# Optimization experiments

Hardware: AMD Instinct MI355X
Metric: run time of the kernel (lower is better)

The kernel has to match this reference:

```python
import jax, jax.numpy as jnp
import numpy as np

VOCAB = 50000
E = 128      # embedding_dim (== hidden so layer weights stack)
H = 128      # hidden_features
L = 2        # n_layers
B = 256      # batch
T = 2048     # seq_len


def setup_inputs() -> dict:
    key = jax.random.key(0)
    ks = jax.random.split(key, 8)
    s = 1.0 / np.sqrt(H)
    x = jax.random.randint(ks[0], (B, T), 0, VOCAB)
    lengths = jax.random.randint(ks[1], (B,), 1, T + 1)
    emb = jax.random.normal(ks[2], (VOCAB, E), jnp.float32) * 0.1
    W_ih = jax.random.uniform(ks[3], (L, H, H), jnp.float32, -s, s)
    W_hh = jax.random.uniform(ks[4], (L, H, H), jnp.float32, -s, s)
    b = jax.random.uniform(ks[5], (L, H), jnp.float32, -s, s)
    cls_w = jax.random.uniform(ks[6], (H, 1), jnp.float32, -s, s)
    cls_b = jnp.zeros((1,), jnp.float32)
    return {"x": x, "lengths": lengths, "emb": emb, "W_ih": W_ih,
            "W_hh": W_hh, "b": b, "cls_w": cls_w, "cls_b": cls_b}


def reference(x, lengths, emb, W_ih, W_hh, b, cls_w, cls_b):
    # x: [B, T] right-padded token ids; lengths: [B] valid lengths.
    ex = emb[x]                       # [B, T, E]
    xs = jnp.moveaxis(ex, 1, 0)       # [T, B, E]
    seq = x.shape[1]
    mask = jnp.arange(seq)[:, None] < lengths[None, :]  # [T, B] alive at step t

    n_layers = W_ih.shape[0]

    def step(hid, inp):
        # hid: [L, B, H]; packed-RNN semantics: only alive rows update.
        tok, m = inp                  # [B, E], [B]
        h_in = tok
        new = []
        for l in range(n_layers):
            h = jnp.tanh(h_in @ W_ih[l] + hid[l] @ W_hh[l] + b[l])
            h = jnp.where(m[:, None], h, hid[l])
            new.append(h)
            h_in = h
        return jnp.stack(new), None

    hid0 = jnp.zeros((n_layers, x.shape[0], W_hh.shape[-1]), emb.dtype)
    hid, _ = jax.lax.scan(step, hid0, (xs, mask))
    # final hidden of last layer -> single-logit sigmoid classifier
    out = jax.nn.sigmoid(hid[-1] @ cls_w + cls_b)  # [B, 1]
    return out
```

## Files before the change

kernel.cpp:

```cpp
#include <hip/hip_runtime.h>
#include <math.h>

#define BATCH 256
#define SEQ   2048
#define HID   128
#define NTHR  256
#define VOCAB 50000

typedef _Float16 v2h __attribute__((ext_vector_type(2)));

template<int CTRL>
__device__ __forceinline__ float dpp_movf(float x) {
    return __builtin_bit_cast(float,
        __builtin_amdgcn_update_dpp(0, __builtin_bit_cast(int, x),
                                    CTRL, 0xF, 0xF, false));
}
__device__ __forceinline__ float quad_reduce(float x) {
    x += dpp_movf<0xB1>(x);
    x += dpp_movf<0x4E>(x);
    return x;
}
__device__ __forceinline__ float fast_rcp(float x) { return __builtin_amdgcn_rcpf(x); }
__device__ __forceinline__ float dot2(v2h a, v2h b, float c) {
    return __builtin_amdgcn_fdot2(a, b, c, false);
}
#define BCH(u) __builtin_bit_cast(v2h, (u))

__device__ __forceinline__ void barrier_lds() {
    asm volatile("s_waitcnt lgkmcnt(0)\n\ts_barrier" ::: "memory");
}

__global__ __launch_bounds__(512, 2) void emb_proj_kernel(
    const float* __restrict__ emb,
    const float* __restrict__ W_ih,
    const float* __restrict__ bias,
    _Float16*    __restrict__ Y)
{
    const int tid  = threadIdx.x;
    const int wave = tid >> 6;
    const int lane = tid & 63;
    const int j    = wave * 16 + (lane >> 2);
    const int q    = lane & 3;

    __shared__ __align__(16) _Float16 xr[HID];

    v2h w[16];
#pragma unroll
    for (int i = 0; i < 16; ++i) {
        const int k = q * 32 + 2 * i;
        w[i] = v2h{(_Float16)W_ih[k * HID + j], (_Float16)W_ih[(k + 1) * HID + j]};
    }
    const float bj = bias[j];
    const float4* embf4 = (const float4*)emb;

    for (int r = blockIdx.x; r < VOCAB; r += gridDim.x) {
        if (tid < 32) {
            float4 v = embf4[(size_t)r * 32 + tid];
            uint a01 = __builtin_bit_cast(uint, __builtin_amdgcn_cvt_pkrtz(v.x, v.y));
            uint a23 = __builtin_bit_cast(uint, __builtin_amdgcn_cvt_pkrtz(v.z, v.w));
            ((uint2*)&xr[0])[tid] = uint2{a01, a23};
        }
        __syncthreads();
        const uint4* xp = (const uint4*)&xr[0] + q * 4;
        float acc = 0.f;
#pragma unroll
        for (int i = 0; i < 4; ++i) {
            const uint4 xu = xp[i];
            acc = dot2(BCH(xu.x), w[4*i+0], acc);
            acc = dot2(BCH(xu.y), w[4*i+1], acc);
            acc = dot2(BCH(xu.z), w[4*i+2], acc);
            acc = dot2(BCH(xu.w), w[4*i+3], acc);
        }
        acc = quad_reduce(acc) + bj;
        if (q == 0) Y[(size_t)r * HID + j] = (_Float16)acc;
        __syncthreads();
    }
}

__global__ __launch_bounds__(NTHR, 1) void rnn_dot2_kernel(
    const int*      __restrict__ x,
    const int*      __restrict__ lengths,
    const _Float16* __restrict__ Y,
    const float*    __restrict__ W_ih,
    const float*    __restrict__ W_hh,
    const float*    __restrict__ bias,
    const float*    __restrict__ cls_w,
    const float*    __restrict__ cls_b,
    float*          __restrict__ out)
{
    const int b    = blockIdx.x;
    const int tid  = threadIdx.x;
    const int wave = tid >> 6;
    const int lane = tid & 63;
    const int jg   = wave * 16 + (lane >> 2);
    const int q    = lane & 3;
    const int jm   = lane & 1;
    const int isl1 = (lane >> 1) & 1;
    const int jt   = 2 * jg + jm;

    __shared__ int xids[SEQ];
    __shared__ __align__(16) _Float16 h0h[2][HID];
    __shared__ __align__(16) _Float16 h1h[2][HID];
    __shared__ __align__(16) float    red[HID];

    const int len   = lengths[b];
    const int lenm1 = len - 1;
    const float LOG2E2 = 2.88539008177793f;

    for (int i = tid; i < SEQ; i += NTHR) xids[i] = x[b * SEQ + i];
    if (tid < HID) {
        h0h[0][tid] = (_Float16)0.f; h0h[1][tid] = (_Float16)0.f;
        h1h[0][tid] = (_Float16)0.f; h1h[1][tid] = (_Float16)0.f;
    }

    v2h whh0[2][16], wih1[2][16], whh1[2][16];
#pragma unroll
    for (int i = 0; i < 16; ++i) {
        const int k = 32 * q + 2 * i;
#pragma unroll
        for (int m = 0; m < 2; ++m) {
            const int j = 2 * jg + m;
            whh0[m][i] = v2h{(_Float16)W_hh[k * HID + j],
                             (_Float16)W_hh[(k + 1) * HID + j]};
            wih1[m][i] = v2h{(_Float16)W_ih[HID * HID + k * HID + j],
                             (_Float16)W_ih[HID * HID + (k + 1) * HID + j]};
            whh1[m][i] = v2h{(_Float16)W_hh[HID * HID + k * HID + j],
                             (_Float16)W_hh[HID * HID + (k + 1) * HID + j]};
        }
    }
    const float b1K = bias[HID + jt] * LOG2E2;

    __syncthreads();

    _Float16 zA = Y[(size_t)xids[0] * HID + jt];
    _Float16 zB = Y[(size_t)xids[min(1, lenm1)] * HID + jt];

    int ph = 0, pf = 0;

#define TANH_PRE(ZK) (1.0f - 2.0f * fast_rcp(__builtin_amdgcn_exp2f(ZK) + 1.0f))

#define DO_PHASE(RD, WR, ZREG)                                              \
    {                                                                       \
        const uint4* h0p = (const uint4*)&h0h[RD][0] + q * 4;               \
        const uint4* h1p = (const uint4*)&h1h[RD][0] + q * 4;               \
        const float zcK = (float)ZREG * LOG2E2;                             \
        {                                                                   \
            const int tn = xids[min(ph + 2, lenm1)];                        \
            ZREG = Y[(size_t)tn * HID + jt];                                \
        }                                                                   \
        float a0_0 = 0.f, a0_1 = 0.f;             \
        float aA_0 = 0.f, aA_1 = 0.f;                        \
        float aB_0 = 0.f, aB_1 = 0.f;                        \
        _Pragma("unroll")                                                   \
        for (int c = 0; c < 4; ++c) {                                       \
            const uint4 hu = h0p[c];                                        \
            const uint4 gu = h1p[c];                                        \
            a0_0 = dot2(BCH(hu.x), whh0[0][4*c+0], a0_0);                   \
            a0_0 = dot2(BCH(hu.y), whh0[0][4*c+1], a0_0);                   \
            a0_0 = dot2(BCH(hu.z), whh0[0][4*c+2], a0_0);                   \
            a0_0 = dot2(BCH(hu.w), whh0[0][4*c+3], a0_0);                   \
            a0_1 = dot2(BCH(hu.x), whh0[1][4*c+0], a0_1);                   \
            a0_1 = dot2(BCH(hu.y), whh0[1][4*c+1], a0_1);                   \
            a0_1 = dot2(BCH(hu.z), whh0[1][4*c+2], a0_1);                   \
            a0_1 = dot2(BCH(hu.w), whh0[1][4*c+3], a0_1);                   \
            aA_0 = dot2(BCH(hu.x), wih1[0][4*c+0], aA_0);                   \
            aA_0 = dot2(BCH(hu.y), wih1[0][4*c+1], aA_0);                   \
            aA_0 = dot2(BCH(hu.z), wih1[0][4*c+2], aA_0);                   \
            aA_0 = dot2(BCH(hu.w), wih1[0][4*c+3], aA_0);                   \
            aA_1 = dot2(BCH(hu.x), wih1[1][4*c+0], aA_1);                   \
            aA_1 = dot2(BCH(hu.y), wih1[1][4*c+1], aA_1);                   \
            aA_1 = dot2(BCH(hu.z), wih1[1][4*c+2], aA_1);                   \
            aA_1 = dot2(BCH(hu.w), wih1[1][4*c+3], aA_1);                   \
            aB_0 = dot2(BCH(gu.x), whh1[0][4*c+0], aB_0);                   \
            aB_0 = dot2(BCH(gu.y), whh1[0][4*c+1], aB_0);                   \
            aB_0 = dot2(BCH(gu.z), whh1[0][4*c+2], aB_0);                   \
            aB_0 = dot2(BCH(gu.w), whh1[0][4*c+3], aB_0);                   \
            aB_1 = dot2(BCH(gu.x), whh1[1][4*c+0], aB_1);                   \
            aB_1 = dot2(BCH(gu.y), whh1[1][4*c+1], aB_1);                   \
            aB_1 = dot2(BCH(gu.z), whh1[1][4*c+2], aB_1);                   \
            aB_1 = dot2(BCH(gu.w), whh1[1][4*c+3], aB_1);                   \
        }                                                                   \
        float s0_0 = quad_reduce(a0_0);                                     \
        float s0_1 = quad_reduce(a0_1);                                     \
        float s1_0 = quad_reduce(aA_0 + aB_0);                              \
        float s1_1 = quad_reduce(aA_1 + aB_1);                              \
        const float sj  = jm  ? (isl1 ? s1_1 : s0_1) : (isl1 ? s1_0 : s0_0);\
        const float cj  = isl1 ? b1K : zcK;                                 \
        const float t   = TANH_PRE(__builtin_fmaf(sj, LOG2E2, cj));         \
        if (!isl1) { if (ph < len) h0h[WR][jt] = (_Float16)t; }             \
        else       { if (ph >= 1)  h1h[WR][jt] = (_Float16)t; }             \
        barrier_lds();                                                      \
    }

    for (;;) {
        DO_PHASE(0, 1, zA)
        ++ph;
        if (ph > len) { pf = 1; break; }
        DO_PHASE(1, 0, zB)
        ++ph;
        if (ph > len) { pf = 0; break; }
    }
#undef DO_PHASE
#undef TANH_PRE

    if (tid < HID) red[tid] = (float)h1h[pf][tid] * cls_w[tid];
    __syncthreads();
    if (tid == 0) {
        float s = 0.f;
        for (int i = 0; i < HID; ++i) s += red[i];
        s += cls_b[0];
        out[b] = fast_rcp(1.0f + __expf(-s));
    }
}

extern "C" void kernel_launch(void* const* d_in, const int* in_sizes, int n_in,
                              void* d_out, int out_size, void* d_ws, size_t ws_size,
                              hipStream_t stream) {
    const int*   x       = (const int*)  d_in[0];
    const int*   lengths = (const int*)  d_in[1];
    const float* emb     = (const float*)d_in[2];
    const float* W_ih    = (const float*)d_in[3];
    const float* W_hh    = (const float*)d_in[4];
    const float* bias    = (const float*)d_in[5];
    const float* cls_w   = (const float*)d_in[6];
    const float* cls_b   = (const float*)d_in[7];
    float*       out     = (float*)      d_out;

    _Float16* Yws = (_Float16*)d_ws;

    emb_proj_kernel<<<2048, 512, 0, stream>>>(emb, W_ih, bias, Yws);
    rnn_dot2_kernel<<<BATCH, NTHR, 0, stream>>>(
        x, lengths, Yws, W_ih, W_hh, bias, cls_w, cls_b, out);
}
```

Before: 834.7 us.

## Split RNN block into layer-0 and layer-1 wave groups with extra pipeline stage

```diff
diff --git a/kernel.cpp b/kernel.cpp
--- a/kernel.cpp
+++ b/kernel.cpp
@@ -4,7 +4,7 @@
 #define BATCH 256
 #define SEQ   2048
 #define HID   128
-#define NTHR  256
+#define NTHR  512
 #define VOCAB 50000
 
 typedef _Float16 v2h __attribute__((ext_vector_type(2)));
@@ -31,10 +31,8 @@
 }
 
 __global__ __launch_bounds__(512, 2) void emb_proj_kernel(
-    const float* __restrict__ emb,
-    const float* __restrict__ W_ih,
-    const float* __restrict__ bias,
-    _Float16*    __restrict__ Y)
+    const float* __restrict__ emb, const float* __restrict__ W_ih,
+    const float* __restrict__ bias, _Float16* __restrict__ Y)
 {
     const int tid  = threadIdx.x;
     const int wave = tid >> 6;
@@ -77,7 +75,7 @@
     }
 }
 
-__global__ __launch_bounds__(NTHR, 1) void rnn_dot2_kernel(
+__global__ __launch_bounds__(NTHR, 1) void rnn_split_kernel(
     const int*      __restrict__ x,
     const int*      __restrict__ lengths,
     const _Float16* __restrict__ Y,
@@ -92,117 +90,160 @@
     const int tid  = threadIdx.x;
     const int wave = tid >> 6;
     const int lane = tid & 63;
-    const int jg   = wave * 16 + (lane >> 2);
+    const bool isA = wave < 4;
+    const int wl   = isA ? wave : (wave - 4);
+    const int jg   = wl * 16 + (lane >> 2);
     const int q    = lane & 3;
     const int jm   = lane & 1;
-    const int isl1 = (lane >> 1) & 1;
+    const int sel  = (lane >> 1) & 1;
     const int jt   = 2 * jg + jm;
 
     __shared__ int xids[SEQ];
     __shared__ __align__(16) _Float16 h0h[2][HID];
     __shared__ __align__(16) _Float16 h1h[2][HID];
+    __shared__ __align__(16) float    gh[2][HID];
     __shared__ __align__(16) float    red[HID];
 
     const int len   = lengths[b];
     const int lenm1 = len - 1;
+    const int LIM   = len + 1;
     const float LOG2E2 = 2.88539008177793f;
 
     for (int i = tid; i < SEQ; i += NTHR) xids[i] = x[b * SEQ + i];
     if (tid < HID) {
         h0h[0][tid] = (_Float16)0.f; h0h[1][tid] = (_Float16)0.f;
         h1h[0][tid] = (_Float16)0.f; h1h[1][tid] = (_Float16)0.f;
-    }
-
-    v2h whh0[2][16], wih1[2][16], whh1[2][16];
-#pragma unroll
-    for (int i = 0; i < 16; ++i) {
-        const int k = 32 * q + 2 * i;
-#pragma unroll
-        for (int m = 0; m < 2; ++m) {
-            const int j = 2 * jg + m;
-            whh0[m][i] = v2h{(_Float16)W_hh[k * HID + j],
-                             (_Float16)W_hh[(k + 1) * HID + j]};
-            wih1[m][i] = v2h{(_Float16)W_ih[HID * HID + k * HID + j],
-                             (_Float16)W_ih[HID * HID + (k + 1) * HID + j]};
-            whh1[m][i] = v2h{(_Float16)W_hh[HID * HID + k * HID + j],
-                             (_Float16)W_hh[HID * HID + (k + 1) * HID + j]};
-        }
-    }
-    const float b1K = bias[HID + jt] * LOG2E2;
-
+        gh[0][tid]  = 0.f;           gh[1][tid]  = 0.f;
+    }
     __syncthreads();
 
-    _Float16 zA = Y[(size_t)xids[0] * HID + jt];
-    _Float16 zB = Y[(size_t)xids[min(1, lenm1)] * HID + jt];
-
     int ph = 0, pf = 0;
 
 #define TANH_PRE(ZK) (1.0f - 2.0f * fast_rcp(__builtin_amdgcn_exp2f(ZK) + 1.0f))
 
-#define DO_PHASE(RD, WR, ZREG)                                              \
+    if (isA) {
+        v2h whh0[2][16], wg[2][16];
+#pragma unroll
+        for (int i = 0; i < 16; ++i) {
+            const int k = 32 * q + 2 * i;
+#pragma unroll
+            for (int m = 0; m < 2; ++m) {
+                const int j = 2 * jg + m;
+                whh0[m][i] = v2h{(_Float16)W_hh[k * HID + j],
+                                 (_Float16)W_hh[(k + 1) * HID + j]};
+                wg[m][i]   = v2h{(_Float16)W_ih[HID * HID + k * HID + j],
+                                 (_Float16)W_ih[HID * HID + (k + 1) * HID + j]};
+            }
+        }
+        _Float16 zA = Y[(size_t)xids[0] * HID + jt];
+        _Float16 zB = Y[(size_t)xids[min(1, lenm1)] * HID + jt];
+
+#define A_PHASE(RD, WR, ZREG)                                               \
     {                                                                       \
         const uint4* h0p = (const uint4*)&h0h[RD][0] + q * 4;               \
-        const uint4* h1p = (const uint4*)&h1h[RD][0] + q * 4;               \
         const float zcK = (float)ZREG * LOG2E2;                             \
         {                                                                   \
             const int tn = xids[min(ph + 2, lenm1)];                        \
             ZREG = Y[(size_t)tn * HID + jt];                                \
         }                                                                   \
-        float a0_0 = 0.f, a0_1 = 0.f;             \
-        float aA_0 = 0.f, aA_1 = 0.f;                        \
-        float aB_0 = 0.f, aB_1 = 0.f;                        \
+        float a0 = 0.f, a1 = 0.f, g0 = 0.f, g1 = 0.f;                       \
         _Pragma("unroll")                                                   \
         for (int c = 0; c < 4; ++c) {                                       \
             const uint4 hu = h0p[c];                                        \
+            a0 = dot2(BCH(hu.x), whh0[0][4*c+0], a0);                       \
+            a0 = dot2(BCH(hu.y), whh0[0][4*c+1], a0);                       \
+            a0 = dot2(BCH(hu.z), whh0[0][4*c+2], a0);                       \
+            a0 = dot2(BCH(hu.w), whh0[0][4*c+3], a0);                       \
+            a1 = dot2(BCH(hu.x), whh0[1][4*c+0], a1);                       \
+            a1 = dot2(BCH(hu.y), whh0[1][4*c+1], a1);                       \
+            a1 = dot2(BCH(hu.z), whh0[1][4*c+2], a1);                       \
+            a1 = dot2(BCH(hu.w), whh0[1][4*c+3], a1);                       \
+            g0 = dot2(BCH(hu.x), wg[0][4*c+0], g0);                         \
+            g0 = dot2(BCH(hu.y), wg[0][4*c+1], g0);                         \
+            g0 = dot2(BCH(hu.z), wg[0][4*c+2], g0);                         \
+            g0 = dot2(BCH(hu.w), wg[0][4*c+3], g0);                         \
+            g1 = dot2(BCH(hu.x), wg[1][4*c+0], g1);                         \
+            g1 = dot2(BCH(hu.y), wg[1][4*c+1], g1);                         \
+            g1 = dot2(BCH(hu.z), wg[1][4*c+2], g1);                         \
+            g1 = dot2(BCH(hu.w), wg[1][4*c+3], g1);                         \
+        }                                                                   \
+        const float r0 = quad_reduce(a0);                                   \
+        const float r1 = quad_reduce(a1);                                   \
+        const float q0 = quad_reduce(g0);                                   \
+        const float q1 = quad_reduce(g1);                                   \
+        if (!sel) {                                                         \
+            const float r = jm ? r1 : r0;                                   \
+            const float t = TANH_PRE(__builtin_fmaf(r, LOG2E2, zcK));       \
+            if (ph < len) h0h[WR][jt] = (_Float16)t;                        \
+        } else {                                                            \
+            gh[WR][jt] = jm ? q1 : q0;                                      \
+        }                                                                   \
+        barrier_lds();                                                      \
+    }
+
+        for (;;) {
+            A_PHASE(0, 1, zA)
+            ++ph;
+            if (ph > LIM) { pf = 1; break; }
+            A_PHASE(1, 0, zB)
+            ++ph;
+            if (ph > LIM) { pf = 0; break; }
+        }
+#undef A_PHASE
+    } else {
+        v2h whh1[2][16];
+#pragma unroll
+        for (int i = 0; i < 16; ++i) {
+            const int k = 32 * q + 2 * i;
+#pragma unroll
+            for (int m = 0; m < 2; ++m) {
+                const int j = 2 * jg + m;
+                whh1[m][i] = v2h{(_Float16)W_hh[HID * HID + k * HID + j],
+                                 (_Float16)W_hh[HID * HID + (k + 1) * HID + j]};
+            }
+        }
+        const float b1K = bias[HID + jt] * LOG2E2;
+
+#define B_PHASE(RD, WR)                                                     \
+    {                                                                       \
+        const uint4* h1p = (const uint4*)&h1h[RD][0] + q * 4;               \
+        const float gvf = gh[RD][jt];                                       \
+        float a0 = 0.f, a1 = 0.f;                                           \
+        _Pragma("unroll")                                                   \
+        for (int c = 0; c < 4; ++c) {                                       \
             const uint4 gu = h1p[c];                                        \
-            a0_0 = dot2(BCH(hu.x), whh0[0][4*c+0], a0_0);                   \
-            a0_0 = dot2(BCH(hu.y), whh0[0][4*c+1], a0_0);                   \
-            a0_0 = dot2(BCH(hu.z), whh0[0][4*c+2], a0_0);                   \
-            a0_0 = dot2(BCH(hu.w), whh0[0][4*c+3], a0_0);                   \
-            a0_1 = dot2(BCH(hu.x), whh0[1][4*c+0], a0_1);                   \
-            a0_1 = dot2(BCH(hu.y), whh0[1][4*c+1], a0_1);                   \
-            a0_1 = dot2(BCH(hu.z), whh0[1][4*c+2], a0_1);                   \
-            a0_1 = dot2(BCH(hu.w), whh0[1][4*c+3], a0_1);                   \
-            aA_0 = dot2(BCH(hu.x), wih1[0][4*c+0], aA_0);                   \
-            aA_0 = dot2(BCH(hu.y), wih1[0][4*c+1], aA_0);                   \
-            aA_0 = dot2(BCH(hu.z), wih1[0][4*c+2], aA_0);                   \
-            aA_0 = dot2(BCH(hu.w), wih1[0][4*c+3], aA_0);                   \
-            aA_1 = dot2(BCH(hu.x), wih1[1][4*c+0], aA_1);                   \
-            aA_1 = dot2(BCH(hu.y), wih1[1][4*c+1], aA_1);                   \
-            aA_1 = dot2(BCH(hu.z), wih1[1][4*c+2], aA_1);                   \
-            aA_1 = dot2(BCH(hu.w), wih1[1][4*c+3], aA_1);                   \
-            aB_0 = dot2(BCH(gu.x), whh1[0][4*c+0], aB_0);                   \
-            aB_0 = dot2(BCH(gu.y), whh1[0][4*c+1], aB_0);                   \
-            aB_0 = dot2(BCH(gu.z), whh1[0][4*c+2], aB_0);                   \
-            aB_0 = dot2(BCH(gu.w), whh1[0][4*c+3], aB_0);                   \
-            aB_1 = dot2(BCH(gu.x), whh1[1][4*c+0], aB_1);                   \
-            aB_1 = dot2(BCH(gu.y), whh1[1][4*c+1], aB_1);                   \
-            aB_1 = dot2(BCH(gu.z), whh1[1][4*c+2], aB_1);                   \
-            aB_1 = dot2(BCH(gu.w), whh1[1][4*c+3], aB_1);                   \
-        }                                                                   \
-        float s0_0 = quad_reduce(a0_0);                                     \
-        float s0_1 = quad_reduce(a0_1);                                     \
-        float s1_0 = quad_reduce(aA_0 + aB_0);                              \
-        float s1_1 = quad_reduce(aA_1 + aB_1);                              \
-        const float sj  = jm  ? (isl1 ? s1_1 : s0_1) : (isl1 ? s1_0 : s0_0);\
-        const float cj  = isl1 ? b1K : zcK;                                 \
-        const float t   = TANH_PRE(__builtin_fmaf(sj, LOG2E2, cj));         \
-        if (!isl1) { if (ph < len) h0h[WR][jt] = (_Float16)t; }             \
-        else       { if (ph >= 1)  h1h[WR][jt] = (_Float16)t; }             \
+            a0 = dot2(BCH(gu.x), whh1[0][4*c+0], a0);                       \
+            a0 = dot2(BCH(gu.y), whh1[0][4*c+1], a0);                       \
+            a0 = dot2(BCH(gu.z), whh1[0][4*c+2], a0);                       \
+            a0 = dot2(BCH(gu.w), whh1[0][4*c+3], a0);                       \
+            a1 = dot2(BCH(gu.x), whh1[1][4*c+0], a1);                       \
+            a1 = dot2(BCH(gu.y), whh1[1][4*c+1], a1);                       \
+            a1 = dot2(BCH(gu.z), whh1[1][4*c+2], a1);                       \
+            a1 = dot2(BCH(gu.w), whh1[1][4*c+3], a1);                       \
+        }                                                                   \
+        const float r0 = quad_reduce(a0);                                   \
+        const float r1 = quad_reduce(a1);                                   \
+        if (!sel) {                                                         \
+            const float r = (jm ? r1 : r0) + gvf;                           \
+            const float t = TANH_PRE(__builtin_fmaf(r, LOG2E2, b1K));       \
+            if (ph >= 2) h1h[WR][jt] = (_Float16)t;                         \
+        }                                                                   \
         barrier_lds();                                                      \
     }
 
-    for (;;) {
-        DO_PHASE(0, 1, zA)
-        ++ph;
-        if (ph > len) { pf = 1; break; }
-        DO_PHASE(1, 0, zB)
-        ++ph;
-        if (ph > len) { pf = 0; break; }
-    }
-#undef DO_PHASE
+        for (;;) {
+            B_PHASE(0, 1)
+            ++ph;
+            if (ph > LIM) { pf = 1; break; }
+            B_PHASE(1, 0)
+            ++ph;
+            if (ph > LIM) { pf = 0; break; }
+        }
+#undef B_PHASE
+    }
 #undef TANH_PRE
 
+    __syncthreads();
     if (tid < HID) red[tid] = (float)h1h[pf][tid] * cls_w[tid];
     __syncthreads();
     if (tid == 0) {
@@ -229,6 +270,6 @@
     _Float16* Yws = (_Float16*)d_ws;
 
     emb_proj_kernel<<<2048, 512, 0, stream>>>(emb, W_ih, bias, Yws);
-    rnn_dot2_kernel<<<BATCH, NTHR, 0, stream>>>(
+    rnn_split_kernel<<<BATCH, NTHR, 0, stream>>>(
         x, lengths, Yws, W_ih, W_hh, bias, cls_w, cls_b, out);
 }
```

Measured after the change: 882.1 us. +5.7%, slower.
